# Kernel optimization log

Hardware: AMD Instinct MI355X
Metric: run time of the kernel (lower is better)

## Reference

```python
import jax, jax.numpy as jnp
import numpy as np

N = 50000
E = 800000
IN_DIM = 128
HIDDEN = 32
HEADS = 4
NUM_CLASSES = 10


def _glorot(key, shape):
    fan_in, fan_out = shape
    lim = float(np.sqrt(6.0 / (fan_in + fan_out)))
    return jax.random.uniform(key, shape, jnp.float32, -lim, lim)


def transformer_conv(x, src, dst, Wq, bq, Wk, bk, Wv, bv, Ws, bs, heads, out_ch, concat):
    """PyG TransformerConv (root_weight=True, beta=False, no edge_attr), eval mode."""
    n = x.shape[0]
    q = (x @ Wq + bq).reshape(n, heads, out_ch)
    k = (x @ Wk + bk).reshape(n, heads, out_ch)
    v = (x @ Wv + bv).reshape(n, heads, out_ch)
    # gather per-edge: query from target i, key/value from source j
    qe = q[dst]                                  # [E, H, C]
    ke = k[src]                                  # [E, H, C]
    ve = v[src]                                  # [E, H, C]
    logits = jnp.einsum('ehc,ehc->eh', qe, ke) / jnp.sqrt(jnp.float32(out_ch))
    # segment softmax over incoming edges of each target node
    m = jax.ops.segment_max(logits, dst, num_segments=n)        # [N, H]
    m = jnp.where(jnp.isfinite(m), m, 0.0)
    e = jnp.exp(logits - m[dst])                                # [E, H]
    denom = jax.ops.segment_sum(e, dst, num_segments=n)         # [N, H]
    alpha = e / (denom[dst] + 1e-16)                            # [E, H]
    agg = jax.ops.segment_sum(alpha[..., None] * ve, dst, num_segments=n)  # [N, H, C]
    if concat:
        out = agg.reshape(n, heads * out_ch)
    else:
        out = agg.mean(axis=1)
    return out + x @ Ws + bs  # root/skip connection


def setup_inputs() -> dict:
    key = jax.random.key(0)
    ks = jax.random.split(key, 20)
    x = jax.random.normal(ks[0], (N, IN_DIM), jnp.float32)
    edge_index = jax.random.randint(ks[1], (2, E), 0, N, jnp.int32)
    d1 = HEADS * HIDDEN  # conv1 per-head stacked width = 128
    params = {
        'Wq1': _glorot(ks[2], (IN_DIM, d1)), 'bq1': jnp.zeros((d1,), jnp.float32),
        'Wk1': _glorot(ks[3], (IN_DIM, d1)), 'bk1': jnp.zeros((d1,), jnp.float32),
        'Wv1': _glorot(ks[4], (IN_DIM, d1)), 'bv1': jnp.zeros((d1,), jnp.float32),
        'Ws1': _glorot(ks[5], (IN_DIM, d1)), 'bs1': jnp.zeros((d1,), jnp.float32),
        'Wq2': _glorot(ks[6], (d1, NUM_CLASSES)), 'bq2': jnp.zeros((NUM_CLASSES,), jnp.float32),
        'Wk2': _glorot(ks[7], (d1, NUM_CLASSES)), 'bk2': jnp.zeros((NUM_CLASSES,), jnp.float32),
        'Wv2': _glorot(ks[8], (d1, NUM_CLASSES)), 'bv2': jnp.zeros((NUM_CLASSES,), jnp.float32),
        'Ws2': _glorot(ks[9], (d1, NUM_CLASSES)), 'bs2': jnp.zeros((NUM_CLASSES,), jnp.float32),
    }
    return {'x': x, 'edge_index': edge_index, **params}


def reference(x, edge_index,
              Wq1, bq1, Wk1, bk1, Wv1, bv1, Ws1, bs1,
              Wq2, bq2, Wk2, bk2, Wv2, bv2, Ws2, bs2):
    src, dst = edge_index[0], edge_index[1]
    h = transformer_conv(x, src, dst, Wq1, bq1, Wk1, bk1, Wv1, bv1, Ws1, bs1,
                         HEADS, HIDDEN, concat=True)
    h = jax.nn.elu(h)
    # dropout is identity in eval mode
    out = transformer_conv(h, src, dst, Wq2, bq2, Wk2, bk2, Wv2, bv2, Ws2, bs2,
                           1, NUM_CLASSES, concat=False)
    return out
```

## Files before the change

kernel.cpp:

```cpp
#include <hip/hip_runtime.h>
#include <hip/hip_fp16.h>
#include <math.h>

#define NN 50000
#define EE 800000
#define NB 196

typedef _Float16 f16x8 __attribute__((ext_vector_type(8)));
typedef float f32x4 __attribute__((ext_vector_type(4)));

__device__ inline float elu1(float x) { return x > 0.f ? x : expm1f(x); }

__global__ __launch_bounds__(256) void build_weights(
    const float* __restrict__ Wq, const float* __restrict__ Wk,
    const float* __restrict__ Wv, const float* __restrict__ Ws,
    const float* __restrict__ Wq2, const float* __restrict__ bq2,
    const float* __restrict__ Wk2, const float* __restrict__ bk2,
    const float* __restrict__ Wv2, const float* __restrict__ bv2,
    const float* __restrict__ Ws2, const float* __restrict__ bs2,
    __half* __restrict__ Wt, __half* __restrict__ W2t, float* __restrict__ bias2)
{
    const int idx = blockIdx.x * 256 + threadIdx.x;
    if (idx < 8192) {
        const int col = idx >> 7, k = idx & 127;
        const int m = col >> 4, j = col & 15;
        const float* W = m == 0 ? Wq2 : m == 1 ? Wk2 : m == 2 ? Wv2 : Ws2;
        W2t[idx] = (__half)(j < 10 ? W[k * 10 + j] : 0.f);
    }
    if (idx < 64) {
        const int m = idx >> 4, j = idx & 15;
        const float* b = m == 0 ? bq2 : m == 1 ? bk2 : m == 2 ? bv2 : bs2;
        bias2[idx] = j < 10 ? b[j] : 0.f;
    }
    __shared__ float tile[32][33];
    const int mat = blockIdx.x >> 4;
    const int tid = blockIdx.x & 15;
    const int k0 = (tid >> 2) * 32, c0 = (tid & 3) * 32;
    const float* W = mat == 0 ? Wq : mat == 1 ? Wk : mat == 2 ? Wv : Ws;
    const int r = threadIdx.x >> 5;
    const int c = threadIdx.x & 31;
    for (int rr = r; rr < 32; rr += 8) tile[rr][c] = W[(size_t)(k0 + rr) * 128 + c0 + c];
    __syncthreads();
    for (int rr = r; rr < 32; rr += 8)
        Wt[((size_t)mat * 128 + c0 + rr) * 128 + k0 + c] = (__half)tile[c][rr];
}

__global__ __launch_bounds__(256) void block_sums(
    const int* __restrict__ deg, int* __restrict__ bsum)
{
    __shared__ int ws[4];
    const int t = threadIdx.x;
    const int idx = blockIdx.x * 256 + t;
    int d = (idx < NN) ? deg[idx] : 0;
    #pragma unroll
    for (int off = 32; off; off >>= 1) d += __shfl_down(d, off, 64);
    if ((t & 63) == 0) ws[t >> 6] = d;
    __syncthreads();
    if (t == 0) bsum[blockIdx.x] = ws[0] + ws[1] + ws[2] + ws[3];
}

__global__ __launch_bounds__(256) void scan_bsums(int* __restrict__ bsum)
{
    __shared__ int s[256];
    const int t = threadIdx.x;
    int v = (t < NB) ? bsum[t] : 0;
    s[t] = v;
    __syncthreads();
    for (int off = 1; off < 256; off <<= 1) {
        int u = (t >= off) ? s[t - off] : 0;
        __syncthreads();
        s[t] += u;
        __syncthreads();
    }
    if (t < NB) bsum[t] = (t == 0) ? 0 : s[t - 1];
}

__global__ __launch_bounds__(256) void write_rowptr(
    const int* __restrict__ deg, const int* __restrict__ bsum,
    int* __restrict__ rowptr, int* __restrict__ cursor)
{
    __shared__ int s[256];
    const int t = threadIdx.x;
    const int idx = blockIdx.x * 256 + t;
    const int d = (idx < NN) ? deg[idx] : 0;
    s[t] = d;
    __syncthreads();
    for (int off = 1; off < 256; off <<= 1) {
        int u = (t >= off) ? s[t - off] : 0;
        __syncthreads();
        s[t] += u;
        __syncthreads();
    }
    const int excl = ((t == 0) ? 0 : s[t - 1]) + bsum[blockIdx.x];
    if (idx < NN) {
        rowptr[idx] = excl;
        cursor[idx] = excl;
    }
    if (idx == NN - 1) rowptr[NN] = excl + d;
}

__global__ __launch_bounds__(256) void scatter_edges(
    const int* __restrict__ src, const int* __restrict__ dst,
    int* __restrict__ cursor, int* __restrict__ esrc)
{
    const int e = blockIdx.x * 256 + threadIdx.x;
    if (e >= EE) return;
    const int d = dst[e];
    const int pos = atomicAdd(&cursor[d], 1);
    esrc[pos] = src[e];
}

__global__ __launch_bounds__(128) void gemm_l1_mfma(
    const float* __restrict__ x, const __half* __restrict__ Wt,
    const float* __restrict__ bq, const float* __restrict__ bk,
    const float* __restrict__ bv, const float* __restrict__ bs,
    const int* __restrict__ dst, int* __restrict__ deg,
    __half* __restrict__ oqh, __half* __restrict__ okh,
    __half* __restrict__ ovh, __half* __restrict__ osh)
{
    const int pair = blockIdx.y;
    const int t = threadIdx.x;

    {
        const int gtid = (blockIdx.y * gridDim.x + blockIdx.x) * 128 + t;
        #pragma unroll
        for (int u = 0; u < 8; ++u) {
            const int e = u * 100096 + gtid;
            if (e < EE) atomicAdd(&deg[dst[e]], 1);
        }
    }

    const int wave = t >> 6;
    const int lane = t & 63;
    const int l = lane & 15;
    const int g = lane >> 4;
    const int wrow0 = blockIdx.x * 128 + wave * 64;
    if (wrow0 >= NN) return;
    const bool full = (wrow0 + 64 <= NN);

    f16x8 xf[4][4];
    #pragma unroll
    for (int rt = 0; rt < 4; ++rt) {
        int arow = wrow0 + rt * 16 + l;
        if (!full && arow >= NN) arow = NN - 1;
        #pragma unroll
        for (int kk = 0; kk < 4; ++kk) {
            const float* xp = x + (size_t)arow * 128 + kk * 32 + g * 8;
            const float4 a = *(const float4*)xp;
            const float4 b = *(const float4*)(xp + 4);
            f16x8 f;
            f[0] = (_Float16)a.x; f[1] = (_Float16)a.y;
            f[2] = (_Float16)a.z; f[3] = (_Float16)a.w;
            f[4] = (_Float16)b.x; f[5] = (_Float16)b.y;
            f[6] = (_Float16)b.z; f[7] = (_Float16)b.w;
            xf[rt][kk] = f;
        }
    }

    for (int mi = 0; mi < 2; ++mi) {
        const int mat = pair * 2 + mi;
        const float* b = mat == 0 ? bq : mat == 1 ? bk : mat == 2 ? bv : bs;
        const _Float16* wt = (const _Float16*)Wt + (size_t)mat * 128 * 128;

        f16x8 wf[4], wfn[4];
        #pragma unroll
        for (int kk = 0; kk < 4; ++kk)
            wf[kk] = *(const f16x8*)(wt + (size_t)l * 128 + kk * 32 + g * 8);

        for (int ct = 0; ct < 8; ++ct) {
            if (ct < 7) {
                const int ncol = (ct + 1) * 16 + l;
                #pragma unroll
                for (int kk = 0; kk < 4; ++kk)
                    wfn[kk] = *(const f16x8*)(wt + (size_t)ncol * 128 + kk * 32 + g * 8);
            }
            f32x4 acc[4];
            #pragma unroll
            for (int rt = 0; rt < 4; ++rt) acc[rt] = (f32x4){0.f, 0.f, 0.f, 0.f};
            #pragma unroll
            for (int kk = 0; kk < 4; ++kk)
                #pragma unroll
                for (int rt = 0; rt < 4; ++rt)
                    acc[rt] = __builtin_amdgcn_mfma_f32_16x16x32_f16(wf[kk], xf[rt][kk], acc[rt], 0, 0, 0);

            const int col0 = ct * 16 + g * 4;
            const float4 bias = *(const float4*)(b + col0);
            __half* o = mat == 0 ? oqh : mat == 1 ? okh : mat == 2 ? ovh : osh;
            #pragma unroll
            for (int rt = 0; rt < 4; ++rt) {
                const int row = wrow0 + rt * 16 + l;
                if (full || row < NN) {
                    __half* p = o + (size_t)row * 128 + col0;
                    *(__half2*)p = __floats2half2_rn(acc[rt][0] + bias.x, acc[rt][1] + bias.y);
                    *(__half2*)(p + 2) = __floats2half2_rn(acc[rt][2] + bias.z, acc[rt][3] + bias.w);
                }
            }
            #pragma unroll
            for (int kk = 0; kk < 4; ++kk) wf[kk] = wfn[kk];
        }
    }
}

__global__ __launch_bounds__(256) void node_attn1(
    const __half* __restrict__ q1, const __half* __restrict__ k1,
    const __half* __restrict__ v1,
    const int* __restrict__ rowptr, const int* __restrict__ esrc,
    const __half* __restrict__ skiph,
    __half* __restrict__ hb)
{
    const int t = threadIdx.x;
    const int wid = __builtin_amdgcn_readfirstlane(t >> 6);
    const int d = blockIdx.x * 4 + wid;
    if (d >= NN) return;
    const int lane = t & 63;
    const int ch2 = lane << 1;

    const int beg = rowptr[d];
    const int end = rowptr[d + 1];

    float2 qv = __half22float2(*(const __half2*)(q1 + (size_t)d * 128 + ch2));
    qv.x *= 0.17677669529663687f;
    qv.y *= 0.17677669529663687f;

    float2 accA = make_float2(0.f, 0.f), accB = make_float2(0.f, 0.f);
    float sA = 0.f, sB = 0.f;

    int i = beg;
    int sa = (i < end) ? esrc[i] : 0;
    int sb = (i + 1 < end) ? esrc[i + 1] : 0;
    __half2 kA = *(const __half2*)(k1 + (size_t)sa * 128 + ch2);
    __half2 vA = *(const __half2*)(v1 + (size_t)sa * 128 + ch2);
    __half2 kB = *(const __half2*)(k1 + (size_t)sb * 128 + ch2);
    __half2 vB = *(const __half2*)(v1 + (size_t)sb * 128 + ch2);

    while (i + 1 < end) {
        const int ni = i + 2;
        const int nsa = (ni < end) ? esrc[ni] : 0;
        const int nsb = (ni + 1 < end) ? esrc[ni + 1] : 0;
        const __half2 nkA = *(const __half2*)(k1 + (size_t)nsa * 128 + ch2);
        const __half2 nvA = *(const __half2*)(v1 + (size_t)nsa * 128 + ch2);
        const __half2 nkB = *(const __half2*)(k1 + (size_t)nsb * 128 + ch2);
        const __half2 nvB = *(const __half2*)(v1 + (size_t)nsb * 128 + ch2);

        const float2 kAf = __half22float2(kA);
        const float2 kBf = __half22float2(kB);
        const float2 vAf = __half22float2(vA);
        const float2 vBf = __half22float2(vB);

        float pA = qv.x * kAf.x + qv.y * kAf.y;
        float pB = qv.x * kBf.x + qv.y * kBf.y;
        pA += __shfl_xor(pA, 8, 16); pB += __shfl_xor(pB, 8, 16);
        pA += __shfl_xor(pA, 4, 16); pB += __shfl_xor(pB, 4, 16);
        pA += __shfl_xor(pA, 2, 16); pB += __shfl_xor(pB, 2, 16);
        pA += __shfl_xor(pA, 1, 16); pB += __shfl_xor(pB, 1, 16);

        const float exA = __expf(pA - 4.0f);
        accA.x += exA * vAf.x;
        accA.y += exA * vAf.y;
        sA += exA;

        const float exB = __expf(pB - 4.0f);
        accB.x += exB * vBf.x;
        accB.y += exB * vBf.y;
        sB += exB;

        kA = nkA; vA = nvA; kB = nkB; vB = nvB;
        i = ni;
    }
    if (i < end) {
        const float2 kAf = __half22float2(kA);
        const float2 vAf = __half22float2(vA);
        float pA = qv.x * kAf.x + qv.y * kAf.y;
        pA += __shfl_xor(pA, 8, 16);
        pA += __shfl_xor(pA, 4, 16);
        pA += __shfl_xor(pA, 2, 16);
        pA += __shfl_xor(pA, 1, 16);
        const float exA = __expf(pA - 4.0f);
        accA.x += exA * vAf.x;
        accA.y += exA * vAf.y;
        sA += exA;
    }

    const float inv = 1.f / (sA + sB + 1e-16f);
    float2 o = __half22float2(*(const __half2*)(skiph + (size_t)d * 128 + ch2));
    o.x = elu1(o.x + (accA.x + accB.x) * inv);
    o.y = elu1(o.y + (accA.y + accB.y) * inv);
    *(__half2*)(hb + (size_t)d * 128 + ch2) = __floats2half2_rn(o.x, o.y);
}

__global__ __launch_bounds__(128) void node_l2_mfma(
    const __half* __restrict__ hb, const __half* __restrict__ W2t,
    const float* __restrict__ bias2,
    __half* __restrict__ q2h, __half* __restrict__ kv2h,
    float* __restrict__ out)
{
    const int t = threadIdx.x;
    const int wave = t >> 6;
    const int lane = t & 63;
    const int l = lane & 15;
    const int g = lane >> 4;
    const int wrow0 = blockIdx.x * 128 + wave * 64;
    if (wrow0 >= NN) return;
    const bool full = (wrow0 + 64 <= NN);

    f16x8 hf[4][4];
    #pragma unroll
    for (int rt = 0; rt < 4; ++rt) {
        int arow = wrow0 + rt * 16 + l;
        if (!full && arow >= NN) arow = NN - 1;
        #pragma unroll
        for (int kk = 0; kk < 4; ++kk)
            hf[rt][kk] = *(const f16x8*)((const _Float16*)hb + (size_t)arow * 128 + kk * 32 + g * 8);
    }

    #pragma unroll
    for (int ct = 0; ct < 4; ++ct) {
        const int col = ct * 16 + l;
        f16x8 wf[4];
        #pragma unroll
        for (int kk = 0; kk < 4; ++kk)
            wf[kk] = *(const f16x8*)((const _Float16*)W2t + (size_t)col * 128 + kk * 32 + g * 8);

        f32x4 acc[4];
        #pragma unroll
        for (int rt = 0; rt < 4; ++rt) acc[rt] = (f32x4){0.f, 0.f, 0.f, 0.f};
        #pragma unroll
        for (int kk = 0; kk < 4; ++kk)
            #pragma unroll
            for (int rt = 0; rt < 4; ++rt)
                acc[rt] = __builtin_amdgcn_mfma_f32_16x16x32_f16(wf[kk], hf[rt][kk], acc[rt], 0, 0, 0);

        const int c0 = g * 4;
        const float4 bias = *(const float4*)(bias2 + ct * 16 + c0);
        #pragma unroll
        for (int rt = 0; rt < 4; ++rt) {
            const int row = wrow0 + rt * 16 + l;
            if (full || row < NN) {
                float4 r;
                r.x = acc[rt][0] + bias.x;
                r.y = acc[rt][1] + bias.y;
                r.z = acc[rt][2] + bias.z;
                r.w = acc[rt][3] + bias.w;
                if (ct == 0) {
                    __half* p = q2h + (size_t)row * 16 + c0;
                    *(__half2*)p = __floats2half2_rn(r.x, r.y);
                    *(__half2*)(p + 2) = __floats2half2_rn(r.z, r.w);
                } else if (ct == 1) {
                    __half* p = kv2h + (size_t)row * 32 + c0;
                    *(__half2*)p = __floats2half2_rn(r.x, r.y);
                    *(__half2*)(p + 2) = __floats2half2_rn(r.z, r.w);
                } else if (ct == 2) {
                    __half* p = kv2h + (size_t)row * 32 + 16 + c0;
                    *(__half2*)p = __floats2half2_rn(r.x, r.y);
                    *(__half2*)(p + 2) = __floats2half2_rn(r.z, r.w);
                } else {
                    if (g < 2) {
                        *(float4*)(out + (size_t)row * 10 + c0) = r;
                    } else if (g == 2) {
                        out[(size_t)row * 10 + 8] = r.x;
                        out[(size_t)row * 10 + 9] = r.y;
                    }
                }
            }
        }
    }
}

__global__ __launch_bounds__(256) void node_attn2(
    const __half* __restrict__ q2h, const __half* __restrict__ kv2h,
    const int* __restrict__ rowptr, const int* __restrict__ esrc,
    float* __restrict__ out)
{
    const int t = threadIdx.x;
    const int d = blockIdx.x * 32 + (t >> 3);
    if (d >= NN) return;
    const int c = t & 7;
    const int beg = rowptr[d];
    const int end = rowptr[d + 1];

    float2 qv = __half22float2(*(const __half2*)(q2h + (size_t)d * 16 + 2 * c));
    qv.x *= 0.31622776601683794f;
    qv.y *= 0.31622776601683794f;

    float2 accA = make_float2(0.f, 0.f), accB = make_float2(0.f, 0.f);
    float sA = 0.f, sB = 0.f;

    int i = beg;
    int sa = (i < end) ? esrc[i] : 0;
    int sb = (i + 1 < end) ? esrc[i + 1] : 0;
    __half2 kA = *(const __half2*)(kv2h + (size_t)sa * 32 + 2 * c);
    __half2 vA = *(const __half2*)(kv2h + (size_t)sa * 32 + 16 + 2 * c);
    __half2 kB = *(const __half2*)(kv2h + (size_t)sb * 32 + 2 * c);
    __half2 vB = *(const __half2*)(kv2h + (size_t)sb * 32 + 16 + 2 * c);

    while (i + 1 < end) {
        const int ni = i + 2;
        const int nsa = (ni < end) ? esrc[ni] : 0;
        const int nsb = (ni + 1 < end) ? esrc[ni + 1] : 0;
        const __half2 nkA = *(const __half2*)(kv2h + (size_t)nsa * 32 + 2 * c);
        const __half2 nvA = *(const __half2*)(kv2h + (size_t)nsa * 32 + 16 + 2 * c);
        const __half2 nkB = *(const __half2*)(kv2h + (size_t)nsb * 32 + 2 * c);
        const __half2 nvB = *(const __half2*)(kv2h + (size_t)nsb * 32 + 16 + 2 * c);

        const float2 kAf = __half22float2(kA);
        const float2 kBf = __half22float2(kB);
        const float2 vAf = __half22float2(vA);
        const float2 vBf = __half22float2(vB);

        float pA = qv.x * kAf.x + qv.y * kAf.y;
        float pB = qv.x * kBf.x + qv.y * kBf.y;
        pA += __shfl_xor(pA, 4, 8); pB += __shfl_xor(pB, 4, 8);
        pA += __shfl_xor(pA, 2, 8); pB += __shfl_xor(pB, 2, 8);
        pA += __shfl_xor(pA, 1, 8); pB += __shfl_xor(pB, 1, 8);

        const float exA = __expf(pA - 2.0f);
        accA.x += exA * vAf.x;
        accA.y += exA * vAf.y;
        sA += exA;

        const float exB = __expf(pB - 2.0f);
        accB.x += exB * vBf.x;
        accB.y += exB * vBf.y;
        sB += exB;

        kA = nkA; vA = nvA; kB = nkB; vB = nvB;
        i = ni;
    }
    if (i < end) {
        const float2 kAf = __half22float2(kA);
        const float2 vAf = __half22float2(vA);
        float pA = qv.x * kAf.x + qv.y * kAf.y;
        pA += __shfl_xor(pA, 4, 8);
        pA += __shfl_xor(pA, 2, 8);
        pA += __shfl_xor(pA, 1, 8);
        const float exA = __expf(pA - 2.0f);
        accA.x += exA * vAf.x;
        accA.y += exA * vAf.y;
        sA += exA;
    }

    if (c < 5) {
        const float inv = 1.f / (sA + sB + 1e-16f);
        float2 o = *(float2*)(out + (size_t)d * 10 + 2 * c);
        o.x += (accA.x + accB.x) * inv;
        o.y += (accA.y + accB.y) * inv;
        *(float2*)(out + (size_t)d * 10 + 2 * c) = o;
    }
}

extern "C" void kernel_launch(void* const* d_in, const int* in_sizes, int n_in,
                              void* d_out, int out_size, void* d_ws, size_t ws_size,
                              hipStream_t stream) {
    const float* x   = (const float*)d_in[0];
    const int*   ei  = (const int*)d_in[1];
    const float* Wq1 = (const float*)d_in[2];  const float* bq1 = (const float*)d_in[3];
    const float* Wk1 = (const float*)d_in[4];  const float* bk1 = (const float*)d_in[5];
    const float* Wv1 = (const float*)d_in[6];  const float* bv1 = (const float*)d_in[7];
    const float* Ws1 = (const float*)d_in[8];  const float* bs1 = (const float*)d_in[9];
    const float* Wq2 = (const float*)d_in[10]; const float* bq2 = (const float*)d_in[11];
    const float* Wk2 = (const float*)d_in[12]; const float* bk2 = (const float*)d_in[13];
    const float* Wv2 = (const float*)d_in[14]; const float* bv2 = (const float*)d_in[15];
    const float* Ws2 = (const float*)d_in[16]; const float* bs2 = (const float*)d_in[17];
    float* out = (float*)d_out;

    const int* src = ei;
    const int* dst = ei + EE;

    __half* q1h   = (__half*)d_ws;
    __half* k1h   = q1h + (size_t)NN * 128;
    __half* v1h   = k1h + (size_t)NN * 128;
    __half* skiph = v1h + (size_t)NN * 128;
    __half* hb    = skiph + (size_t)NN * 128;
    __half* Wt    = hb + (size_t)NN * 128;
    __half* W2t   = Wt + 4 * 128 * 128;
    __half* q2h   = W2t + 64 * 128;
    __half* kv2h  = q2h + (size_t)NN * 16;
    float* bias2  = (float*)(kv2h + (size_t)NN * 32);
    int* deg      = (int*)(bias2 + 64);
    int* rowptr   = deg + NN;
    int* cursor   = rowptr + NN + 1;
    int* bsum     = cursor + NN;
    int* esrc     = bsum + NB;

    hipMemsetAsync(deg, 0, (size_t)NN * sizeof(int), stream);
    build_weights<<<64, 256, 0, stream>>>(Wq1, Wk1, Wv1, Ws1,
                                          Wq2, bq2, Wk2, bk2, Wv2, bv2, Ws2, bs2,
                                          Wt, W2t, bias2);

    gemm_l1_mfma<<<dim3((NN + 127) / 128, 2), 128, 0, stream>>>(
        x, Wt, bq1, bk1, bv1, bs1, dst, deg, q1h, k1h, v1h, skiph);

    block_sums<<<NB, 256, 0, stream>>>(deg, bsum);
    scan_bsums<<<1, 256, 0, stream>>>(bsum);
    write_rowptr<<<NB, 256, 0, stream>>>(deg, bsum, rowptr, cursor);
    scatter_edges<<<EE / 256, 256, 0, stream>>>(src, dst, cursor, esrc);

    node_attn1<<<NN / 4, 256, 0, stream>>>(q1h, k1h, v1h, rowptr, esrc, skiph, hb);

    node_l2_mfma<<<(NN + 127) / 128, 128, 0, stream>>>(hb, W2t, bias2, q2h, kv2h, out);

    node_attn2<<<(NN + 31) / 32, 256, 0, stream>>>(q2h, kv2h, rowptr, esrc, out);
}
```

Measured before the change: 219.8 us.

## Split degree counting out of layer-1 GEMM and give each matrix its own block

Degree counting moves out of the layer-1 MFMA GEMM into a separate deg_count kernel. The GEMM grid now has one block row per weight matrix (4 instead of 2), so each block does one matrix and the grid holds more blocks. Output stores are merged into single 8-byte stores in both GEMMs, and the GEMM launch moves after the CSR build. The cost is an extra kernel launch, and the x tile is now loaded and converted four times instead of twice.

```diff
diff --git a/kernel.cpp b/kernel.cpp
--- a/kernel.cpp
+++ b/kernel.cpp
@@ -45,6 +45,14 @@
         Wt[((size_t)mat * 128 + c0 + rr) * 128 + k0 + c] = (__half)tile[c][rr];
 }
 
+__global__ __launch_bounds__(256) void deg_count(
+    const int* __restrict__ dst, int* __restrict__ deg)
+{
+    const int e = blockIdx.x * 256 + threadIdx.x;
+    if (e >= EE) return;
+    atomicAdd(&deg[dst[e]], 1);
+}
+
 __global__ __launch_bounds__(256) void block_sums(
     const int* __restrict__ deg, int* __restrict__ bsum)
 {
@@ -114,22 +122,11 @@
     const float* __restrict__ x, const __half* __restrict__ Wt,
     const float* __restrict__ bq, const float* __restrict__ bk,
     const float* __restrict__ bv, const float* __restrict__ bs,
-    const int* __restrict__ dst, int* __restrict__ deg,
     __half* __restrict__ oqh, __half* __restrict__ okh,
     __half* __restrict__ ovh, __half* __restrict__ osh)
 {
-    const int pair = blockIdx.y;
-    const int t = threadIdx.x;
-
-    {
-        const int gtid = (blockIdx.y * gridDim.x + blockIdx.x) * 128 + t;
-        #pragma unroll
-        for (int u = 0; u < 8; ++u) {
-            const int e = u * 100096 + gtid;
-            if (e < EE) atomicAdd(&deg[dst[e]], 1);
-        }
-    }
-
+    const int mat = blockIdx.y;
+    const int t = threadIdx.x;
     const int wave = t >> 6;
     const int lane = t & 63;
     const int l = lane & 15;
@@ -157,47 +154,47 @@
         }
     }
 
-    for (int mi = 0; mi < 2; ++mi) {
-        const int mat = pair * 2 + mi;
-        const float* b = mat == 0 ? bq : mat == 1 ? bk : mat == 2 ? bv : bs;
-        const _Float16* wt = (const _Float16*)Wt + (size_t)mat * 128 * 128;
-
-        f16x8 wf[4], wfn[4];
-        #pragma unroll
-        for (int kk = 0; kk < 4; ++kk)
-            wf[kk] = *(const f16x8*)(wt + (size_t)l * 128 + kk * 32 + g * 8);
-
-        for (int ct = 0; ct < 8; ++ct) {
-            if (ct < 7) {
-                const int ncol = (ct + 1) * 16 + l;
-                #pragma unroll
-                for (int kk = 0; kk < 4; ++kk)
-                    wfn[kk] = *(const f16x8*)(wt + (size_t)ncol * 128 + kk * 32 + g * 8);
-            }
-            f32x4 acc[4];
-            #pragma unroll
-            for (int rt = 0; rt < 4; ++rt) acc[rt] = (f32x4){0.f, 0.f, 0.f, 0.f};
+    const float* b = mat == 0 ? bq : mat == 1 ? bk : mat == 2 ? bv : bs;
+    __half* o = mat == 0 ? oqh : mat == 1 ? okh : mat == 2 ? ovh : osh;
+    const _Float16* wt = (const _Float16*)Wt + (size_t)mat * 128 * 128;
+
+    f16x8 wf[4], wfn[4];
+    #pragma unroll
+    for (int kk = 0; kk < 4; ++kk)
+        wf[kk] = *(const f16x8*)(wt + (size_t)l * 128 + kk * 32 + g * 8);
+
+    for (int ct = 0; ct < 8; ++ct) {
+        if (ct < 7) {
+            const int ncol = (ct + 1) * 16 + l;
             #pragma unroll
             for (int kk = 0; kk < 4; ++kk)
-                #pragma unroll
-                for (int rt = 0; rt < 4; ++rt)
-                    acc[rt] = __builtin_amdgcn_mfma_f32_16x16x32_f16(wf[kk], xf[rt][kk], acc[rt], 0, 0, 0);
-
-            const int col0 = ct * 16 + g * 4;
-            const float4 bias = *(const float4*)(b + col0);
-            __half* o = mat == 0 ? oqh : mat == 1 ? okh : mat == 2 ? ovh : osh;
+                wfn[kk] = *(const f16x8*)(wt + (size_t)ncol * 128 + kk * 32 + g * 8);
+        }
+        f32x4 acc[4];
+        #pragma unroll
+        for (int rt = 0; rt < 4; ++rt) acc[rt] = (f32x4){0.f, 0.f, 0.f, 0.f};
+        #pragma unroll
+        for (int kk = 0; kk < 4; ++kk)
             #pragma unroll
-            for (int rt = 0; rt < 4; ++rt) {
-                const int row = wrow0 + rt * 16 + l;
-                if (full || row < NN) {
-                    __half* p = o + (size_t)row * 128 + col0;
-                    *(__half2*)p = __floats2half2_rn(acc[rt][0] + bias.x, acc[rt][1] + bias.y);
-                    *(__half2*)(p + 2) = __floats2half2_rn(acc[rt][2] + bias.z, acc[rt][3] + bias.w);
-                }
+            for (int rt = 0; rt < 4; ++rt)
+                acc[rt] = __builtin_amdgcn_mfma_f32_16x16x32_f16(wf[kk], xf[rt][kk], acc[rt], 0, 0, 0);
+
+        const int col0 = ct * 16 + g * 4;
+        const float4 bias = *(const float4*)(b + col0);
+        #pragma unroll
+        for (int rt = 0; rt < 4; ++rt) {
+            const int row = wrow0 + rt * 16 + l;
+            if (full || row < NN) {
+                __half2 h01 = __floats2half2_rn(acc[rt][0] + bias.x, acc[rt][1] + bias.y);
+                __half2 h23 = __floats2half2_rn(acc[rt][2] + bias.z, acc[rt][3] + bias.w);
+                uint2 u;
+                u.x = *(unsigned*)&h01;
+                u.y = *(unsigned*)&h23;
+                *(uint2*)(o + (size_t)row * 128 + col0) = u;
             }
-            #pragma unroll
-            for (int kk = 0; kk < 4; ++kk) wf[kk] = wfn[kk];
         }
+        #pragma unroll
+        for (int kk = 0; kk < 4; ++kk) wf[kk] = wfn[kk];
     }
 }
 
@@ -341,25 +338,22 @@
                 r.y = acc[rt][1] + bias.y;
                 r.z = acc[rt][2] + bias.z;
                 r.w = acc[rt][3] + bias.w;
-                if (ct == 0) {
-                    __half* p = q2h + (size_t)row * 16 + c0;
-                    *(__half2*)p = __floats2half2_rn(r.x, r.y);
-                    *(__half2*)(p + 2) = __floats2half2_rn(r.z, r.w);
-                } else if (ct == 1) {
-                    __half* p = kv2h + (size_t)row * 32 + c0;
-                    *(__half2*)p = __floats2half2_rn(r.x, r.y);
-                    *(__half2*)(p + 2) = __floats2half2_rn(r.z, r.w);
-                } else if (ct == 2) {
-                    __half* p = kv2h + (size_t)row * 32 + 16 + c0;
-                    *(__half2*)p = __floats2half2_rn(r.x, r.y);
-                    *(__half2*)(p + 2) = __floats2half2_rn(r.z, r.w);
-                } else {
+                if (ct == 3) {
                     if (g < 2) {
                         *(float4*)(out + (size_t)row * 10 + c0) = r;
                     } else if (g == 2) {
                         out[(size_t)row * 10 + 8] = r.x;
                         out[(size_t)row * 10 + 9] = r.y;
                     }
+                } else {
+                    __half* p = ct == 0 ? q2h + (size_t)row * 16 + c0
+                              : kv2h + (size_t)row * 32 + (ct == 2 ? 16 : 0) + c0;
+                    __half2 h01 = __floats2half2_rn(r.x, r.y);
+                    __half2 h23 = __floats2half2_rn(r.z, r.w);
+                    uint2 u;
+                    u.x = *(unsigned*)&h01;
+                    u.y = *(unsigned*)&h23;
+                    *(uint2*)p = u;
                 }
             }
         }
@@ -483,18 +477,18 @@
     int* esrc     = bsum + NB;
 
     hipMemsetAsync(deg, 0, (size_t)NN * sizeof(int), stream);
+    deg_count<<<EE / 256, 256, 0, stream>>>(dst, deg);
     build_weights<<<64, 256, 0, stream>>>(Wq1, Wk1, Wv1, Ws1,
                                           Wq2, bq2, Wk2, bk2, Wv2, bv2, Ws2, bs2,
                                           Wt, W2t, bias2);
-
-    gemm_l1_mfma<<<dim3((NN + 127) / 128, 2), 128, 0, stream>>>(
-        x, Wt, bq1, bk1, bv1, bs1, dst, deg, q1h, k1h, v1h, skiph);
-
     block_sums<<<NB, 256, 0, stream>>>(deg, bsum);
     scan_bsums<<<1, 256, 0, stream>>>(bsum);
     write_rowptr<<<NB, 256, 0, stream>>>(deg, bsum, rowptr, cursor);
     scatter_edges<<<EE / 256, 256, 0, stream>>>(src, dst, cursor, esrc);
 
+    gemm_l1_mfma<<<dim3((NN + 127) / 128, 4), 128, 0, stream>>>(
+        x, Wt, bq1, bk1, bv1, bs1, q1h, k1h, v1h, skiph);
+
     node_attn1<<<NN / 4, 256, 0, stream>>>(q1h, k1h, v1h, rowptr, esrc, skiph, hb);
 
     node_l2_mfma<<<(NN + 127) / 128, 128, 0, stream>>>(hb, W2t, bias2, q2h, kv2h, out);
```

Measured after the change: 233.1 us. 1.06x slower.
